# Performance work log

Hardware: AMD Instinct MI355X
Metric: run time of the kernel (lower is better)

## Reference

```python
import jax, jax.numpy as jnp
import numpy as np

N, E, D, H = 50000, 800000, 64, 4


def setup_inputs() -> dict:
    key = jax.random.key(0)
    ks = jax.random.split(key, 12)
    w = lambda k, shape: jax.random.normal(k, shape, jnp.float32) * 0.05
    return {
        "nfeats": jax.random.normal(ks[0], (N, D), jnp.float32),
        "efeats": jax.random.normal(ks[1], (E, D), jnp.float32),
        "src": jax.random.randint(ks[2], (E,), 0, N),
        "dst": jax.random.randint(ks[3], (E,), 0, N),
        "W_ni": w(ks[4], (D, H * D)),
        "W_nj": w(ks[5], (D, H * D)),
        "W_fij": w(ks[6], (D, H * D)),
        "bias_e": jnp.zeros((H * D,), jnp.float32),
        "attn": w(ks[7], (H, D)),
        "W_src": w(ks[8], (D, H * D)),
        "W_mlp_node": w(ks[9], (H * D, D)),
        "b_mlp_node": jnp.zeros((D,), jnp.float32),
        "W_mlp_edge": w(ks[10], (H * D, D)),
        "b_mlp_edge": jnp.zeros((D,), jnp.float32),
    }


def reference(nfeats, efeats, src, dst, W_ni, W_nj, W_fij, bias_e, attn,
              W_src, W_mlp_node, b_mlp_node, W_mlp_edge, b_mlp_edge):
    n, d = nfeats.shape
    h = attn.shape[0]
    # DGL EGATConv: edge logits from src node, dst node and edge features
    f_ni = (nfeats @ W_ni)[src]            # [E, H*D] gather src
    f_nj = (nfeats @ W_nj)[dst]            # [E, H*D] gather dst
    f_fij = efeats @ W_fij                 # [E, H*D]
    f_out = jax.nn.leaky_relu(f_ni + f_nj + f_fij + bias_e, 0.01)
    f_out = f_out.reshape(-1, h, d)        # [E, H, D] new edge feats
    e = jnp.einsum('ehd,hd->eh', f_out, attn)  # [E, H] attention logits
    # edge softmax over incoming edges of each dst node
    e_max = jax.ops.segment_max(e, dst, num_segments=n)
    e_exp = jnp.exp(e - e_max[dst])
    denom = jax.ops.segment_sum(e_exp, dst, num_segments=n)
    a = e_exp / denom[dst]                 # [E, H]
    # weighted message passing: scatter-sum to dst
    h_src = (nfeats @ W_src).reshape(n, h, d)[src]  # [E, H, D]
    h_out = jax.ops.segment_sum(h_src * a[:, :, None], dst, num_segments=n)  # [N, H, D]
    # EGATLayer head-mixing MLPs + ELU
    node = jax.nn.elu(h_out.reshape(n, h * d) @ W_mlp_node + b_mlp_node)
    edge = jax.nn.elu(f_out.reshape(-1, h * d) @ W_mlp_edge + b_mlp_edge)
    return node, edge
```

## Files before the change

kernel.cpp:

```cpp
#include <hip/hip_runtime.h>
#include <hip/hip_bf16.h>

#define N_NODES 50000
#define N_EDGES 800000
#define DD 64
#define HH 4
#define HD 256
#define EB 32
#define CAP 64

typedef __attribute__((ext_vector_type(8))) short bf16x8;
typedef __attribute__((ext_vector_type(4))) float f32x4;

__device__ __forceinline__ short f2bf(float x) {
  return __builtin_bit_cast(short, __float2bfloat16(x));
}
__device__ __forceinline__ float bf2f(unsigned short u) {
  return __builtin_bit_cast(float, (unsigned)u << 16);
}

__global__ __launch_bounds__(256) void k_proj(const float* __restrict__ nfeats,
    const float* __restrict__ W_src, unsigned short* __restrict__ hsrc) {
  __shared__ __align__(16) float Wl[DD * HD];
  const float4* W4 = (const float4*)W_src;
  float4* Wl4 = (float4*)Wl;
#pragma unroll
  for (int i = 0; i < 16; ++i) Wl4[threadIdx.x + i * 256] = W4[threadIdx.x + i * 256];
  __syncthreads();
  const int wave = threadIdx.x >> 6, lane = threadIdx.x & 63;
  for (int n = blockIdx.x * 4 + wave; n < N_NODES; n += gridDim.x * 4) {
    const float4* x4 = (const float4*)(nfeats + n * DD);
    float4 acc = make_float4(0.f, 0.f, 0.f, 0.f);
#pragma unroll
    for (int k4 = 0; k4 < 16; ++k4) {
      float4 xv = x4[k4];
      const float* wr = &Wl[(k4 * 4) * HD + 4 * lane];
      float4 w0 = *(const float4*)(wr);
      float4 w1 = *(const float4*)(wr + HD);
      float4 w2 = *(const float4*)(wr + 2 * HD);
      float4 w3 = *(const float4*)(wr + 3 * HD);
      acc.x += xv.x * w0.x + xv.y * w1.x + xv.z * w2.x + xv.w * w3.x;
      acc.y += xv.x * w0.y + xv.y * w1.y + xv.z * w2.y + xv.w * w3.y;
      acc.z += xv.x * w0.z + xv.y * w1.z + xv.z * w2.z + xv.w * w3.z;
      acc.w += xv.x * w0.w + xv.y * w1.w + xv.z * w2.w + xv.w * w3.w;
    }
    short4 s;
    s.x = f2bf(acc.x); s.y = f2bf(acc.y); s.z = f2bf(acc.z); s.w = f2bf(acc.w);
    *(short4*)&hsrc[n * HD + 4 * lane] = s;
  }
}

__global__ __launch_bounds__(256, 2) void k_edge(
    const float* __restrict__ efeats, const int* __restrict__ src, const int* __restrict__ dst,
    const float* __restrict__ nfeats,
    const float* __restrict__ W_fij, const float* __restrict__ W_ni, const float* __restrict__ W_nj,
    const float* __restrict__ bias_e, const float* __restrict__ attn,
    const float* __restrict__ W_mlp_edge, const float* __restrict__ b_mlp_edge,
    float* __restrict__ eexp, float* __restrict__ edge_out) {
  __shared__ __align__(16) short a_lds[12 * 64 * 8];
  __shared__ __align__(16) short fout_lds[EB * HD];

  const int t = threadIdx.x;
  const int lane = t & 63;
  const int w = t >> 6;
  const int l15 = lane & 15, l4 = lane >> 4;

  bf16x8 wcat[6][4];
#pragma unroll
  for (int ks = 0; ks < 6; ++ks) {
    const float* Wp = ks < 2 ? (W_fij + (ks * 32) * HD)
                             : (ks < 4 ? (W_ni + ((ks - 2) * 32) * HD)
                                       : (W_nj + ((ks - 4) * 32) * HD));
#pragma unroll
    for (int n = 0; n < 4; ++n) {
      bf16x8 a;
#pragma unroll
      for (int i = 0; i < 8; ++i)
        a[i] = f2bf(Wp[(l4 * 8 + i) * HD + (w * 64 + n * 16 + l15)]);
      wcat[ks][n] = a;
    }
  }
  bf16x8 wm[8];
#pragma unroll
  for (int ks = 0; ks < 8; ++ks) {
    bf16x8 b;
#pragma unroll
    for (int i = 0; i < 8; ++i)
      b[i] = f2bf(W_mlp_edge[(ks * 32 + l4 * 8 + i) * 64 + (w * 16 + l15)]);
    wm[ks] = b;
  }
  float bias_r[4], attn_r[4];
#pragma unroll
  for (int n = 0; n < 4; ++n) {
    const int col = w * 64 + n * 16 + l15;
    bias_r[n] = bias_e[col];
    attn_r[n] = attn[col];
  }
  const float bme_r = b_mlp_edge[w * 16 + l15];

  const int fr = t >> 3;
  const int c = t & 7;
  const int fc = c * 8;
  const int msub = fr >> 4, rr = fr & 15, kq = c >> 2, kk = c & 3;
  const int posx = ((rr ^ c) & 15) | (kk << 4);

  for (int tile = blockIdx.x; tile < N_EDGES / EB; tile += gridDim.x) {
    const int base = tile * EB;
    {
      const int srow = src[base + fr], drow = dst[base + fr];
      float4 x0, x1; bf16x8 p;

      x0 = *(const float4*)&efeats[(base + fr) * DD + fc];
      x1 = *(const float4*)&efeats[(base + fr) * DD + fc + 4];
      p[0] = f2bf(x0.x); p[1] = f2bf(x0.y); p[2] = f2bf(x0.z); p[3] = f2bf(x0.w);
      p[4] = f2bf(x1.x); p[5] = f2bf(x1.y); p[6] = f2bf(x1.z); p[7] = f2bf(x1.w);
      ((bf16x8*)a_lds)[(msub * 6 + kq) * 64 + posx] = p;

      x0 = *(const float4*)&nfeats[srow * DD + fc];
      x1 = *(const float4*)&nfeats[srow * DD + fc + 4];
      p[0] = f2bf(x0.x); p[1] = f2bf(x0.y); p[2] = f2bf(x0.z); p[3] = f2bf(x0.w);
      p[4] = f2bf(x1.x); p[5] = f2bf(x1.y); p[6] = f2bf(x1.z); p[7] = f2bf(x1.w);
      ((bf16x8*)a_lds)[(msub * 6 + 2 + kq) * 64 + posx] = p;

      x0 = *(const float4*)&nfeats[drow * DD + fc];
      x1 = *(const float4*)&nfeats[drow * DD + fc + 4];
      p[0] = f2bf(x0.x); p[1] = f2bf(x0.y); p[2] = f2bf(x0.z); p[3] = f2bf(x0.w);
      p[4] = f2bf(x1.x); p[5] = f2bf(x1.y); p[6] = f2bf(x1.z); p[7] = f2bf(x1.w);
      ((bf16x8*)a_lds)[(msub * 6 + 4 + kq) * 64 + posx] = p;
    }
    __syncthreads();

    f32x4 acc[2][4] = {};
#pragma unroll
    for (int m = 0; m < 2; ++m) {
      bf16x8 af[6];
#pragma unroll
      for (int ks = 0; ks < 6; ++ks) {
        const int px = (((lane & 15) ^ (((ks & 1) << 2) | (lane >> 4))) & 15) | ((lane >> 4) << 4);
        af[ks] = ((const bf16x8*)a_lds)[(m * 6 + ks) * 64 + px];
      }
#pragma unroll
      for (int n = 0; n < 4; ++n)
#pragma unroll
        for (int ks = 0; ks < 6; ++ks)
          acc[m][n] = __builtin_amdgcn_mfma_f32_16x16x32_bf16(af[ks], wcat[ks][n], acc[m][n], 0, 0, 0);
    }

#pragma unroll
    for (int m = 0; m < 2; ++m) {
#pragma unroll
      for (int reg = 0; reg < 4; ++reg) {
        const int re = m * 16 + l4 * 4 + reg;
        float p = 0.f;
#pragma unroll
        for (int n = 0; n < 4; ++n) {
          const int col = w * 64 + n * 16 + l15;
          float v = acc[m][n][reg] + bias_r[n];
          v = v >= 0.f ? v : 0.01f * v;
          p += v * attn_r[n];
          int byte = re * 512 + col * 2;
          byte ^= (re & 7) << 4;
          *(short*)((char*)fout_lds + byte) = f2bf(v);
        }
        p += __shfl_xor(p, 1, 64); p += __shfl_xor(p, 2, 64);
        p += __shfl_xor(p, 4, 64); p += __shfl_xor(p, 8, 64);
        if (l15 == 0) {
          eexp[(base + re) * 4 + w] = expf(p);
        }
      }
    }
    __syncthreads();

#pragma unroll
    for (int m = 0; m < 2; ++m) {
      f32x4 acc2 = {};
#pragma unroll
      for (int ks = 0; ks < 8; ++ks) {
        int byte = (m * 16 + l15) * 512 + ks * 64 + l4 * 16;
        byte ^= (l15 & 7) << 4;
        bf16x8 pf = *(const bf16x8*)((char*)fout_lds + byte);
        acc2 = __builtin_amdgcn_mfma_f32_16x16x32_bf16(pf, wm[ks], acc2, 0, 0, 0);
      }
#pragma unroll
      for (int reg = 0; reg < 4; ++reg) {
        float v = acc2[reg] + bme_r;
        v = v > 0.f ? v : (expf(v) - 1.f);
        edge_out[(size_t)(base + m * 16 + l4 * 4 + reg) * DD + w * 16 + l15] = v;
      }
    }
  }
}

__global__ __launch_bounds__(256) void k_fill(const int* __restrict__ dst,
    int* __restrict__ cnt, int* __restrict__ bucket) {
  const int e = blockIdx.x * 256 + threadIdx.x;
  if (e < N_EDGES) {
    const int d = dst[e];
    const int slot = atomicAdd(&cnt[d], 1);
    if (slot < CAP) bucket[d * CAP + slot] = e;
  }
}

__global__ __launch_bounds__(256) void k_aggf(const int* __restrict__ src,
    const int* __restrict__ cnt, const int* __restrict__ bucket,
    const float* __restrict__ eexp, const unsigned short* __restrict__ hsrc_all,
    const float* __restrict__ W_mlp_node, const float* __restrict__ b_mlp_node,
    float* __restrict__ node_out) {
  __shared__ __align__(16) float h_lds[4][256];
  __shared__ float part[4][4][64];
  const int lane = threadIdx.x & 63;
  const int q = threadIdx.x >> 6;
  bf16x8 wn8[8];
#pragma unroll
  for (int i = 0; i < 8; ++i) {
    bf16x8 v;
#pragma unroll
    for (int j = 0; j < 8; ++j) v[j] = f2bf(W_mlp_node[(q * 64 + i * 8 + j) * 64 + lane]);
    wn8[i] = v;
  }
  const float br = b_mlp_node[lane];
  const int hq = lane >> 4;

  for (int nb = blockIdx.x * 4; nb < N_NODES; nb += gridDim.x * 4) {
    const int n = nb + q;
    int deg = 0;
    float ex0 = 0.f, ex1 = 0.f, ex2 = 0.f, ex3 = 0.f;
    int s = 0;
    if (n < N_NODES) {
      deg = cnt[n];
      if (deg > CAP) deg = CAP;
      if (lane < deg) {
        const int e = bucket[n * CAP + lane];
        s = src[e];
        const float4 ex = *(const float4*)&eexp[e * 4];
        ex0 = ex.x; ex1 = ex.y; ex2 = ex.z; ex3 = ex.w;
      }
    }
    float d0 = ex0, d1 = ex1, d2 = ex2, d3 = ex3;
#pragma unroll
    for (int off = 32; off; off >>= 1) {
      d0 += __shfl_xor(d0, off, 64); d1 += __shfl_xor(d1, off, 64);
      d2 += __shfl_xor(d2, off, 64); d3 += __shfl_xor(d3, off, 64);
    }
    const float dsel = hq == 0 ? d0 : hq == 1 ? d1 : hq == 2 ? d2 : d3;
    const float inv = dsel > 0.f ? 1.f / dsel : 0.f;
    float4 a4 = make_float4(0.f, 0.f, 0.f, 0.f);
    for (int i = 0; i < deg; ++i) {
      const int si = __shfl(s, i, 64);
      const float w0 = __shfl(ex0, i, 64), w1 = __shfl(ex1, i, 64);
      const float w2 = __shfl(ex2, i, 64), w3 = __shfl(ex3, i, 64);
      const float wsel = hq == 0 ? w0 : hq == 1 ? w1 : hq == 2 ? w2 : w3;
      const ushort4 v = *(const ushort4*)&hsrc_all[(size_t)si * HD + lane * 4];
      a4.x += wsel * bf2f(v.x);
      a4.y += wsel * bf2f(v.y);
      a4.z += wsel * bf2f(v.z);
      a4.w += wsel * bf2f(v.w);
    }
    float4 h4;
    h4.x = a4.x * inv; h4.y = a4.y * inv; h4.z = a4.z * inv; h4.w = a4.w * inv;
    *(float4*)&h_lds[q][lane * 4] = h4;
    __syncthreads();
#pragma unroll
    for (int j = 0; j < 4; ++j) {
      float out = 0.f;
#pragma unroll
      for (int i = 0; i < 8; ++i)
#pragma unroll
        for (int jj = 0; jj < 8; ++jj)
          out += h_lds[j][q * 64 + i * 8 + jj] * bf2f((unsigned short)wn8[i][jj]);
      part[j][q][lane] = out;
    }
    __syncthreads();
    {
      const int nj = nb + q;
      if (nj < N_NODES) {
        float v = part[q][0][lane] + part[q][1][lane] + part[q][2][lane] + part[q][3][lane] + br;
        v = v > 0.f ? v : (expf(v) - 1.f);
        node_out[(size_t)nj * DD + lane] = v;
      }
    }
  }
}

extern "C" void kernel_launch(void* const* d_in, const int* in_sizes, int n_in,
                              void* d_out, int out_size, void* d_ws, size_t ws_size,
                              hipStream_t stream) {
  const float* nfeats     = (const float*)d_in[0];
  const float* efeats     = (const float*)d_in[1];
  const int*   src        = (const int*)d_in[2];
  const int*   dst        = (const int*)d_in[3];
  const float* W_ni       = (const float*)d_in[4];
  const float* W_nj       = (const float*)d_in[5];
  const float* W_fij      = (const float*)d_in[6];
  const float* bias_e     = (const float*)d_in[7];
  const float* attn       = (const float*)d_in[8];
  const float* W_src      = (const float*)d_in[9];
  const float* W_mlp_node = (const float*)d_in[10];
  const float* b_mlp_node = (const float*)d_in[11];
  const float* W_mlp_edge = (const float*)d_in[12];
  const float* b_mlp_edge = (const float*)d_in[13];

  float* node_out = (float*)d_out;
  float* edge_out = node_out + (size_t)N_NODES * DD;

  char* wsb = (char*)d_ws;
  unsigned short* hsrc_bf = (unsigned short*)wsb;
  float* eexp   = (float*)(wsb + 25600000);
  int*   cnt    = (int*)(wsb + 89600000);
  int*   bucket = (int*)(wsb + 89800000);

  hipMemsetAsync(cnt, 0, (size_t)N_NODES * sizeof(int), stream);
  k_proj<<<512, 256, 0, stream>>>(nfeats, W_src, hsrc_bf);
  k_edge<<<1024, 256, 0, stream>>>(efeats, src, dst, nfeats,
                                   W_fij, W_ni, W_nj, bias_e, attn,
                                   W_mlp_edge, b_mlp_edge, eexp, edge_out);
  k_fill<<<(N_EDGES + 255) / 256, 256, 0, stream>>>(dst, cnt, bucket);
  k_aggf<<<2048, 256, 0, stream>>>(src, cnt, bucket, eexp, hsrc_bf,
                                   W_mlp_node, b_mlp_node, node_out);
}
```

Baseline: 562.4 us.

## Merge projection, edge, and bucket-fill kernels into one block-partitioned launch

Combines the node projection, edge compute, and dst-bucket fill kernels into a single launch and dispatches on block index ranges, so the three independent stages run concurrently and two kernel boundaries go away. Every block now reserves 64KB of unified shared memory, including the fill blocks that use none. This can lower occupancy for the edge and fill work. The kernel also inherits the edge kernel's launch bounds and register pressure for all roles.

```diff
diff --git a/kernel.cpp b/kernel.cpp
--- a/kernel.cpp
+++ b/kernel.cpp
@@ -8,6 +8,9 @@
 #define HD 256
 #define EB 32
 #define CAP 64
+#define EDGE_BLKS 1024
+#define PROJ_BLKS 512
+#define FILL_BLKS ((N_EDGES + 255) / 256)
 
 typedef __attribute__((ext_vector_type(8))) short bf16x8;
 typedef __attribute__((ext_vector_type(4))) float f32x4;
@@ -19,46 +22,61 @@
   return __builtin_bit_cast(float, (unsigned)u << 16);
 }
 
-__global__ __launch_bounds__(256) void k_proj(const float* __restrict__ nfeats,
-    const float* __restrict__ W_src, unsigned short* __restrict__ hsrc) {
-  __shared__ __align__(16) float Wl[DD * HD];
-  const float4* W4 = (const float4*)W_src;
-  float4* Wl4 = (float4*)Wl;
-#pragma unroll
-  for (int i = 0; i < 16; ++i) Wl4[threadIdx.x + i * 256] = W4[threadIdx.x + i * 256];
-  __syncthreads();
-  const int wave = threadIdx.x >> 6, lane = threadIdx.x & 63;
-  for (int n = blockIdx.x * 4 + wave; n < N_NODES; n += gridDim.x * 4) {
-    const float4* x4 = (const float4*)(nfeats + n * DD);
-    float4 acc = make_float4(0.f, 0.f, 0.f, 0.f);
-#pragma unroll
-    for (int k4 = 0; k4 < 16; ++k4) {
-      float4 xv = x4[k4];
-      const float* wr = &Wl[(k4 * 4) * HD + 4 * lane];
-      float4 w0 = *(const float4*)(wr);
-      float4 w1 = *(const float4*)(wr + HD);
-      float4 w2 = *(const float4*)(wr + 2 * HD);
-      float4 w3 = *(const float4*)(wr + 3 * HD);
-      acc.x += xv.x * w0.x + xv.y * w1.x + xv.z * w2.x + xv.w * w3.x;
-      acc.y += xv.x * w0.y + xv.y * w1.y + xv.z * w2.y + xv.w * w3.y;
-      acc.z += xv.x * w0.z + xv.y * w1.z + xv.z * w2.z + xv.w * w3.z;
-      acc.w += xv.x * w0.w + xv.y * w1.w + xv.z * w2.w + xv.w * w3.w;
-    }
-    short4 s;
-    s.x = f2bf(acc.x); s.y = f2bf(acc.y); s.z = f2bf(acc.z); s.w = f2bf(acc.w);
-    *(short4*)&hsrc[n * HD + 4 * lane] = s;
-  }
-}
-
-__global__ __launch_bounds__(256, 2) void k_edge(
+__global__ __launch_bounds__(256, 2) void k_main(
     const float* __restrict__ efeats, const int* __restrict__ src, const int* __restrict__ dst,
     const float* __restrict__ nfeats,
     const float* __restrict__ W_fij, const float* __restrict__ W_ni, const float* __restrict__ W_nj,
     const float* __restrict__ bias_e, const float* __restrict__ attn,
     const float* __restrict__ W_mlp_edge, const float* __restrict__ b_mlp_edge,
-    float* __restrict__ eexp, float* __restrict__ edge_out) {
-  __shared__ __align__(16) short a_lds[12 * 64 * 8];
-  __shared__ __align__(16) short fout_lds[EB * HD];
+    const float* __restrict__ W_src,
+    float* __restrict__ eexp, float* __restrict__ edge_out,
+    unsigned short* __restrict__ hsrc, int* __restrict__ cnt, int* __restrict__ bucket) {
+  __shared__ __align__(16) char smem[65536];
+
+  if (blockIdx.x >= EDGE_BLKS + PROJ_BLKS) {
+    const int e = (blockIdx.x - EDGE_BLKS - PROJ_BLKS) * 256 + threadIdx.x;
+    if (e < N_EDGES) {
+      const int d = dst[e];
+      const int slot = atomicAdd(&cnt[d], 1);
+      if (slot < CAP) bucket[d * CAP + slot] = e;
+    }
+    return;
+  }
+
+  if (blockIdx.x >= EDGE_BLKS) {
+    float* Wl = (float*)smem;
+    const int bp = blockIdx.x - EDGE_BLKS;
+    const float4* W4 = (const float4*)W_src;
+    float4* Wl4 = (float4*)Wl;
+#pragma unroll
+    for (int i = 0; i < 16; ++i) Wl4[threadIdx.x + i * 256] = W4[threadIdx.x + i * 256];
+    __syncthreads();
+    const int wave = threadIdx.x >> 6, lane = threadIdx.x & 63;
+    for (int n = bp * 4 + wave; n < N_NODES; n += PROJ_BLKS * 4) {
+      const float4* x4 = (const float4*)(nfeats + n * DD);
+      float4 acc = make_float4(0.f, 0.f, 0.f, 0.f);
+#pragma unroll
+      for (int k4 = 0; k4 < 16; ++k4) {
+        float4 xv = x4[k4];
+        const float* wr = &Wl[(k4 * 4) * HD + 4 * lane];
+        float4 w0 = *(const float4*)(wr);
+        float4 w1 = *(const float4*)(wr + HD);
+        float4 w2 = *(const float4*)(wr + 2 * HD);
+        float4 w3 = *(const float4*)(wr + 3 * HD);
+        acc.x += xv.x * w0.x + xv.y * w1.x + xv.z * w2.x + xv.w * w3.x;
+        acc.y += xv.x * w0.y + xv.y * w1.y + xv.z * w2.y + xv.w * w3.y;
+        acc.z += xv.x * w0.z + xv.y * w1.z + xv.z * w2.z + xv.w * w3.z;
+        acc.w += xv.x * w0.w + xv.y * w1.w + xv.z * w2.w + xv.w * w3.w;
+      }
+      short4 s;
+      s.x = f2bf(acc.x); s.y = f2bf(acc.y); s.z = f2bf(acc.z); s.w = f2bf(acc.w);
+      *(short4*)&hsrc[n * HD + 4 * lane] = s;
+    }
+    return;
+  }
+
+  short* a_lds = (short*)smem;
+  short* fout_lds = (short*)(smem + 12288);
 
   const int t = threadIdx.x;
   const int lane = t & 63;
@@ -104,7 +122,7 @@
   const int msub = fr >> 4, rr = fr & 15, kq = c >> 2, kk = c & 3;
   const int posx = ((rr ^ c) & 15) | (kk << 4);
 
-  for (int tile = blockIdx.x; tile < N_EDGES / EB; tile += gridDim.x) {
+  for (int tile = blockIdx.x; tile < N_EDGES / EB; tile += EDGE_BLKS) {
     const int base = tile * EB;
     {
       const int srow = src[base + fr], drow = dst[base + fr];
@@ -188,16 +206,6 @@
         edge_out[(size_t)(base + m * 16 + l4 * 4 + reg) * DD + w * 16 + l15] = v;
       }
     }
-  }
-}
-
-__global__ __launch_bounds__(256) void k_fill(const int* __restrict__ dst,
-    int* __restrict__ cnt, int* __restrict__ bucket) {
-  const int e = blockIdx.x * 256 + threadIdx.x;
-  if (e < N_EDGES) {
-    const int d = dst[e];
-    const int slot = atomicAdd(&cnt[d], 1);
-    if (slot < CAP) bucket[d * CAP + slot] = e;
   }
 }
 
@@ -310,11 +318,9 @@
   int*   bucket = (int*)(wsb + 89800000);
 
   hipMemsetAsync(cnt, 0, (size_t)N_NODES * sizeof(int), stream);
-  k_proj<<<512, 256, 0, stream>>>(nfeats, W_src, hsrc_bf);
-  k_edge<<<1024, 256, 0, stream>>>(efeats, src, dst, nfeats,
-                                   W_fij, W_ni, W_nj, bias_e, attn,
-                                   W_mlp_edge, b_mlp_edge, eexp, edge_out);
-  k_fill<<<(N_EDGES + 255) / 256, 256, 0, stream>>>(dst, cnt, bucket);
+  k_main<<<EDGE_BLKS + PROJ_BLKS + FILL_BLKS, 256, 0, stream>>>(
+      efeats, src, dst, nfeats, W_fij, W_ni, W_nj, bias_e, attn,
+      W_mlp_edge, b_mlp_edge, W_src, eexp, edge_out, hsrc_bf, cnt, bucket);
   k_aggf<<<2048, 256, 0, stream>>>(src, cnt, bucket, eexp, hsrc_bf,
                                    W_mlp_node, b_mlp_node, node_out);
 }
```

Measured after the change: 1.134 ms. +101.6%, slower.
